# Kernel optimization log

Hardware: AMD Instinct MI355X
Metric: run time of the kernel (lower is better)

Reference implementation:

```python
import jax, jax.numpy as jnp
import numpy as np

B, L, D, K, MAXL = 2, 1024, 256, 64, 1024
EPS = 1e-5

def _encode(x, pos, w1, b1, w2, b2, wa, ba):
    # x: [B,L,D] -> complex phasors [B,L,K]
    xa = x + pos[: x.shape[1]][None]
    h = jax.nn.gelu(xa @ w1 + b1, approximate=False)
    phase = jnp.tanh(h @ w2 + b2) * np.float32(np.pi)
    amp = jax.nn.softplus(xa @ wa + ba) + np.float32(0.1)
    return (amp * jnp.exp(1j * phase)).astype(jnp.complex64)

def setup_inputs() -> dict:
    key = jax.random.key(0)
    ks = jax.random.split(key, 24)
    def lin_w(k, i, o):
        return (jax.random.normal(k, (i, o), jnp.float32) / np.sqrt(np.float32(i)))
    def pos(k):
        return jax.random.normal(k, (MAXL, D), jnp.float32) * np.float32(0.02)
    inp = {
        'x': jax.random.normal(ks[0], (B, L, D), jnp.float32),
        'pos_k': pos(ks[1]),
        'w1_k': lin_w(ks[2], D, D), 'b1_k': jnp.zeros((D,), jnp.float32),
        'w2_k': lin_w(ks[3], D, K), 'b2_k': jnp.zeros((K,), jnp.float32),
        'wa_k': lin_w(ks[4], D, K), 'ba_k': jnp.zeros((K,), jnp.float32),
        'pos_q': pos(ks[5]),
        'w1_q': lin_w(ks[6], D, D), 'b1_q': jnp.zeros((D,), jnp.float32),
        'w2_q': lin_w(ks[7], D, K), 'b2_q': jnp.zeros((K,), jnp.float32),
        'wa_q': lin_w(ks[8], D, K), 'ba_q': jnp.zeros((K,), jnp.float32),
        'wv': lin_w(ks[9], D, D), 'bv': jnp.zeros((D,), jnp.float32),
        'ln_g': jnp.ones((D,), jnp.float32), 'ln_b': jnp.zeros((D,), jnp.float32),
        'wo': lin_w(ks[10], D, D), 'bo': jnp.zeros((D,), jnp.float32),
    }
    return inp

def reference(x, pos_k, w1_k, b1_k, w2_k, b2_k, wa_k, ba_k,
              pos_q, w1_q, b1_q, w2_q, b2_q, wa_q, ba_q,
              wv, bv, ln_g, ln_b, wo, bo):
    Bx, Lx, Dx = x.shape
    kp = _encode(x, pos_k, w1_k, b1_k, w2_k, b2_k, wa_k, ba_k)  # [B,L,K] complex
    qp = _encode(x, pos_q, w1_q, b1_q, w2_q, b2_q, wa_q, ba_q)  # [B,L,K] complex
    V = (x @ wv + bv).astype(jnp.complex64)                      # [B,L,D]
    bound = kp[:, :, :, None] * V[:, :, None, :]                 # [B,L,K,D]
    memory = jnp.cumsum(bound, axis=1)                           # [B,L,K,D]
    retrieved = jnp.real(jnp.einsum('blkd,blk->bld', memory, jnp.conj(qp)))
    positions = jnp.arange(1, Lx + 1, dtype=jnp.float32)
    norm = jnp.sqrt(positions * np.float32(kp.shape[-1]))[None, :, None]
    r = retrieved / norm
    mu = jnp.mean(r, axis=-1, keepdims=True)
    var = jnp.var(r, axis=-1, keepdims=True)
    rn = (r - mu) / jnp.sqrt(var + np.float32(EPS)) * ln_g + ln_b
    return x + rn @ wo + bo
```

## Files before the change

kernel.cpp:

```cpp
#include <hip/hip_runtime.h>
#include <hip/hip_bf16.h>

typedef __attribute__((ext_vector_type(8))) short short8;
typedef __attribute__((ext_vector_type(4))) float float4v;

constexpr int B = 2, L = 1024, D = 256, K = 64;
constexpr int N = B * L;
constexpr int NC = L / 64;

constexpr int WT2_OFF = 524288;

__device__ __forceinline__ ushort bf16_hi(float v) {
  return (ushort)(__float_as_uint(v) >> 16);
}
__device__ __forceinline__ float hi_f(float v) {
  return __uint_as_float(__float_as_uint(v) & 0xFFFF0000u);
}
__device__ __forceinline__ ushort bf16_rne(float v) {
  uint b = __float_as_uint(v);
  b += 0x7FFF + ((b >> 16) & 1);
  return (ushort)(b >> 16);
}

__global__ __launch_bounds__(256) void prep_kernel(
    const float* __restrict__ w1_k, const float* __restrict__ w1_q,
    const float* __restrict__ wv, const float* __restrict__ wo,
    const float* __restrict__ w2_k, const float* __restrict__ wa_k,
    const float* __restrict__ w2_q, const float* __restrict__ wa_q,
    ushort* __restrict__ WT) {
  __shared__ float Lt[64][65];
  const int bi = blockIdx.x, tid = threadIdx.x;
  const float* src;
  int ncols, k0, n0;
  ushort* dhi;
  int losz;
  if (bi < 64) {
    const int m = bi >> 4, t = bi & 15;
    src = (m == 0) ? w1_k : (m == 1) ? w1_q : (m == 2) ? wv : wo;
    ncols = 256; k0 = (t >> 2) * 64; n0 = (t & 3) * 64;
    dhi = WT + m * 131072; losz = 65536;
  } else {
    const int m = (bi - 64) >> 2, kt = (bi - 64) & 3;
    src = (m == 0) ? w2_k : (m == 1) ? wa_k : (m == 2) ? w2_q : wa_q;
    ncols = 64; k0 = kt * 64; n0 = 0;
    dhi = WT + WT2_OFF + m * 32768; losz = 16384;
  }
  ushort* dlo = dhi + losz;
  for (int p = 0; p < 16; ++p) {
    const int kr = p * 4 + (tid >> 6), nc = tid & 63;
    Lt[kr][nc] = src[(k0 + kr) * ncols + n0 + nc];
  }
  __syncthreads();
  const int n = tid >> 2, kq = tid & 3;
  uint uh[8], ul[8];
  for (int i = 0; i < 8; ++i) {
    const float v0 = Lt[kq * 16 + 2 * i][n];
    const float v1 = Lt[kq * 16 + 2 * i + 1][n];
    uh[i] = (uint)bf16_hi(v0) | ((uint)bf16_hi(v1) << 16);
    ul[i] = (uint)bf16_rne(v0 - hi_f(v0)) | ((uint)bf16_rne(v1 - hi_f(v1)) << 16);
  }
  const int oidx = (n0 + n) * 256 + k0 + kq * 16;
  *(uint4*)&dhi[oidx] = make_uint4(uh[0], uh[1], uh[2], uh[3]);
  *(uint4*)&dhi[oidx + 8] = make_uint4(uh[4], uh[5], uh[6], uh[7]);
  *(uint4*)&dlo[oidx] = make_uint4(ul[0], ul[1], ul[2], ul[3]);
  *(uint4*)&dlo[oidx + 8] = make_uint4(ul[4], ul[5], ul[6], ul[7]);
}

__global__ __launch_bounds__(256) void enc1_kernel(
    const float* __restrict__ x, const float* __restrict__ pos_k,
    const float* __restrict__ pos_q,
    const float* __restrict__ b1_k, const float* __restrict__ b1_q,
    const float* __restrict__ bv, const ushort* __restrict__ WT,
    float* __restrict__ hk, float* __restrict__ hq, float* __restrict__ V) {
  __shared__ __align__(16) ushort Ah[32][40], Al[32][40];
  __shared__ __align__(16) ushort Bh[64][40], Bl[64][40];
  const int tid = threadIdx.x;
  const int g = blockIdx.x / 256;
  const int rem = blockIdx.x % 256;
  const int row0 = (rem >> 2) * 32, nb = (rem & 3) * 64;
  const float* pos = (g == 0) ? pos_k : (g == 1) ? pos_q : nullptr;
  const ushort* Wh = WT + g * 131072;
  const ushort* Wl = Wh + 65536;
  const int w = tid >> 6, lane = tid & 63;
  const int m16 = lane & 15, quad = lane >> 4;

  float4v acc[2] = {};

  for (int k0 = 0; k0 < 256; k0 += 32) {
    __syncthreads();
    {
      const int r = tid >> 3, kc = (tid & 7) * 4;
      const int row = row0 + r, l = row & (L - 1);
      float4 xv = *(const float4*)&x[row * D + k0 + kc];
      if (pos) {
        const float4 pv = *(const float4*)&pos[l * D + k0 + kc];
        xv.x += pv.x; xv.y += pv.y; xv.z += pv.z; xv.w += pv.w;
      }
      ushort4 h4, l4;
      h4.x = bf16_hi(xv.x); l4.x = bf16_rne(xv.x - hi_f(xv.x));
      h4.y = bf16_hi(xv.y); l4.y = bf16_rne(xv.y - hi_f(xv.y));
      h4.z = bf16_hi(xv.z); l4.z = bf16_rne(xv.z - hi_f(xv.z));
      h4.w = bf16_hi(xv.w); l4.w = bf16_rne(xv.w - hi_f(xv.w));
      *(ushort4*)&Ah[r][kc] = h4;
      *(ushort4*)&Al[r][kc] = l4;
    }
    {
      const int n = tid >> 2, chunk = tid & 3;
      const int ga = (nb + n) * 256 + k0 + chunk * 8;
      *(uint4*)&Bh[n][chunk * 8] = *(const uint4*)&Wh[ga];
      *(uint4*)&Bl[n][chunk * 8] = *(const uint4*)&Wl[ga];
    }
    __syncthreads();

    short8 afh[2], afl[2];
#pragma unroll
    for (int r = 0; r < 2; ++r) {
      afh[r] = *(const short8*)&Ah[r * 16 + m16][quad * 8];
      afl[r] = *(const short8*)&Al[r * 16 + m16][quad * 8];
    }
    const int col = w * 16 + m16;
    const short8 bfh = *(const short8*)&Bh[col][quad * 8];
    const short8 bfl = *(const short8*)&Bl[col][quad * 8];
#pragma unroll
    for (int r = 0; r < 2; ++r) {
      acc[r] = __builtin_amdgcn_mfma_f32_16x16x32_bf16(afh[r], bfh, acc[r], 0, 0, 0);
      acc[r] = __builtin_amdgcn_mfma_f32_16x16x32_bf16(afh[r], bfl, acc[r], 0, 0, 0);
      acc[r] = __builtin_amdgcn_mfma_f32_16x16x32_bf16(afl[r], bfh, acc[r], 0, 0, 0);
    }
  }

  float* outp = (g == 0) ? hk : (g == 1) ? hq : V;
  const float* bp = (g == 0) ? b1_k : (g == 1) ? b1_q : bv;
  const int colg = nb + w * 16 + m16;
  const float bias = bp[colg];
#pragma unroll
  for (int r = 0; r < 2; ++r)
#pragma unroll
    for (int j = 0; j < 4; ++j) {
      const int rowg = row0 + r * 16 + quad * 4 + j;
      float v = acc[r][j] + bias;
      if (g < 2) v = 0.5f * v * (1.0f + erff(v * 0.70710678f));
      outp[rowg * D + colg] = v;
    }
}

__global__ __launch_bounds__(512) void enc2_kernel(
    const float* __restrict__ x, const float* __restrict__ pos_k,
    const float* __restrict__ pos_q, const float* __restrict__ hk,
    const float* __restrict__ hq,
    const float* __restrict__ b2_k, const float* __restrict__ ba_k,
    const float* __restrict__ b2_q, const float* __restrict__ ba_q,
    const ushort* __restrict__ WT,
    float* __restrict__ kr, float* __restrict__ ki,
    float* __restrict__ qr, float* __restrict__ qi) {
  __shared__ __align__(16) ushort Ahh[16][40], Ahl[16][40], Axh[16][40], Axl[16][40];
  __shared__ __align__(16) ushort B2h[64][40], B2l[64][40], Bah[64][40], Bal[64][40];
  __shared__ float phL[16][68], amL[16][68];
  const int tid = threadIdx.x;
  const int e = blockIdx.x >> 7;
  const int r0g = (blockIdx.x & 127) * 16;
  const float* hsrc = e ? hq : hk;
  const float* pos = e ? pos_q : pos_k;
  const ushort* W2h = WT + WT2_OFF + (e ? 2 : 0) * 32768;
  const ushort* W2l = W2h + 16384;
  const ushort* Wah = WT + WT2_OFF + (e ? 3 : 1) * 32768;
  const ushort* Wal = Wah + 16384;
  const int w = tid >> 6, lane = tid & 63;
  const int m16 = lane & 15, quad = lane >> 4;
  const int mat = w & 1, ct = w >> 1;

  float4v acc = {};
  for (int k0 = 0; k0 < 256; k0 += 32) {
    __syncthreads();
    {
      const int half = tid >> 8;
      const int t2 = tid & 255;
      const int r = t2 >> 4, kc = (t2 & 15) * 2;
      const int row = r0g + r, l = row & (L - 1);
      if (half == 0) {
        const float2 hv = *(const float2*)&hsrc[row * D + k0 + kc];
        ushort2 h2, l2;
        h2.x = bf16_hi(hv.x); l2.x = bf16_rne(hv.x - hi_f(hv.x));
        h2.y = bf16_hi(hv.y); l2.y = bf16_rne(hv.y - hi_f(hv.y));
        *(ushort2*)&Ahh[r][kc] = h2;
        *(ushort2*)&Ahl[r][kc] = l2;
      } else {
        const float2 xv = *(const float2*)&x[row * D + k0 + kc];
        const float2 pv = *(const float2*)&pos[l * D + k0 + kc];
        const float a0 = xv.x + pv.x, a1 = xv.y + pv.y;
        ushort2 h2, l2;
        h2.x = bf16_hi(a0); l2.x = bf16_rne(a0 - hi_f(a0));
        h2.y = bf16_hi(a1); l2.y = bf16_rne(a1 - hi_f(a1));
        *(ushort2*)&Axh[r][kc] = h2;
        *(ushort2*)&Axl[r][kc] = l2;
      }
    }
    {
      const int sel = tid >> 7;
      const int idx = tid & 127;
      const int n = idx >> 1, ch = (idx & 1) * 2;
      const int ga = n * 256 + k0 + ch * 8;
      const ushort* s = (sel == 0) ? W2h : (sel == 1) ? W2l : (sel == 2) ? Wah : Wal;
      ushort* dst = (sel == 0) ? &B2h[n][ch * 8] : (sel == 1) ? &B2l[n][ch * 8]
                  : (sel == 2) ? &Bah[n][ch * 8] : &Bal[n][ch * 8];
      *(uint4*)dst = *(const uint4*)&s[ga];
      *(uint4*)(dst + 8) = *(const uint4*)&s[ga + 8];
    }
    __syncthreads();

    const short8 ah = mat ? *(const short8*)&Axh[m16][quad * 8]
                          : *(const short8*)&Ahh[m16][quad * 8];
    const short8 al = mat ? *(const short8*)&Axl[m16][quad * 8]
                          : *(const short8*)&Ahl[m16][quad * 8];
    const int col = ct * 16 + m16;
    const short8 bh = mat ? *(const short8*)&Bah[col][quad * 8]
                          : *(const short8*)&B2h[col][quad * 8];
    const short8 bl = mat ? *(const short8*)&Bal[col][quad * 8]
                          : *(const short8*)&B2l[col][quad * 8];
    acc = __builtin_amdgcn_mfma_f32_16x16x32_bf16(ah, bh, acc, 0, 0, 0);
    acc = __builtin_amdgcn_mfma_f32_16x16x32_bf16(ah, bl, acc, 0, 0, 0);
    acc = __builtin_amdgcn_mfma_f32_16x16x32_bf16(al, bh, acc, 0, 0, 0);
  }

  {
    const int colk = ct * 16 + m16;
    if (mat == 0) {
      const float b2v = (e ? b2_q : b2_k)[colk];
#pragma unroll
      for (int j = 0; j < 4; ++j)
        phL[quad * 4 + j][colk] = tanhf(acc[j] + b2v) * 3.14159265358979f;
    } else {
      const float bav = (e ? ba_q : ba_k)[colk];
#pragma unroll
      for (int j = 0; j < 4; ++j) {
        const float av = acc[j] + bav;
        amL[quad * 4 + j][colk] = fmaxf(av, 0.0f) + log1pf(expf(-fabsf(av))) + 0.1f;
      }
    }
  }
  __syncthreads();
  {
    float* pr = e ? qr : kr;
    float* pim = e ? qi : ki;
#pragma unroll
    for (int p = 0; p < 2; ++p) {
      const int idx = p * 512 + tid;
      const int r = idx >> 6, ccol = idx & 63;
      const int row = r0g + r;
      const float a = amL[r][ccol], pph = phL[r][ccol];
      pr[row * K + ccol] = a * cosf(pph);
      pim[row * K + ccol] = a * sinf(pph);
    }
  }
}

__global__ __launch_bounds__(256) void tbuild_kernel(
    const float* __restrict__ kr, const float* __restrict__ ki,
    const float* __restrict__ V, float* __restrict__ TMt) {
  const int id = blockIdx.x;
  const int dc = id & 15, c = (id >> 4) & 15, b = id >> 8;
  const int tid = threadIdx.x;
  const int n0 = b * L + c * 64;
  const int dl = tid & 15;
  const int kb = tid >> 4;

  __shared__ float krL[64][68], kiL[64][68];
  __shared__ float VL[64][20];
  __shared__ float Tl[16][204];
  for (int e = tid; e < 1024; e += 256) {
    const int t = e >> 4, k4 = (e & 15) * 4;
    *(float4*)&krL[t][k4] = *(const float4*)&kr[(n0 + t) * K + k4];
    *(float4*)&kiL[t][k4] = *(const float4*)&ki[(n0 + t) * K + k4];
  }
  {
    const int t = tid >> 2, f = (tid & 3) * 4;
    *(float4*)&VL[t][f] = *(const float4*)&V[(n0 + t) * D + dc * 16 + f];
  }
  __syncthreads();

  {
    const int t0 = (tid >> 4) * 4;
#pragma unroll
    for (int i = 0; i < 4; ++i) Tl[dl][128 + t0 + i] = VL[t0 + i][dl];
  }

  float ar[4] = {0.f, 0.f, 0.f, 0.f}, ai[4] = {0.f, 0.f, 0.f, 0.f};
#pragma unroll 4
  for (int t = 0; t < 64; ++t) {
    const float vt = VL[t][dl];
    const float4 k4r = *(const float4*)&krL[t][kb * 4];
    const float4 k4i = *(const float4*)&kiL[t][kb * 4];
    ar[0] += k4r.x * vt; ar[1] += k4r.y * vt; ar[2] += k4r.z * vt; ar[3] += k4r.w * vt;
    ai[0] += k4i.x * vt; ai[1] += k4i.y * vt; ai[2] += k4i.z * vt; ai[3] += k4i.w * vt;
  }

#pragma unroll
  for (int i = 0; i < 4; ++i) {
    Tl[dl][kb * 4 + i] = ar[i];
    Tl[dl][64 + kb * 4 + i] = ai[i];
  }
  __syncthreads();

  float* dst = &TMt[(((size_t)(b * 16 + c)) * 256 + dc * 16) * 192];
#pragma unroll
  for (int p = 0; p < 3; ++p) {
    const int e = p * 256 + tid;
    const int row = e / 48, f4 = e % 48;
    *(float4*)&dst[(size_t)row * 192 + f4 * 4] = *(const float4*)&Tl[row][f4 * 4];
  }
}

__global__ __launch_bounds__(512) void ret_kernel(
    const float* __restrict__ qr, const float* __restrict__ qi,
    const float* __restrict__ kr, const float* __restrict__ ki,
    const float* __restrict__ TMt, float* __restrict__ ret,
    float* __restrict__ LNred) {
  __shared__ __align__(16) ushort Ah[64][200], Al[64][200];
  __shared__ __align__(16) ushort Kh[64][136], Kl[64][136];
  __shared__ __align__(16) ushort Bh[32][200], Bl[32][200];
  const int tid = threadIdx.x;
  const int dc = blockIdx.x & 7;
  const int c = (blockIdx.x >> 3) & 15;
  const int b = blockIdx.x >> 7;
  const int n0 = b * L + c * 64;
  const int cols0 = dc * 32;
  const int w = tid >> 6, lane = tid & 63;
  const int m16 = lane & 15, quad = lane >> 4;

#pragma unroll
  for (int j = 0; j < 4; ++j) {
    const int e = j * 512 + tid;
    const int row = e >> 5, c4 = e & 31;
    const int col0 = (c4 & 15) * 4;
    const int acol = (c4 < 16 ? 0 : 64) + col0;
    {
      const float* src = (c4 < 16) ? qr : qi;
      const float4 v = *(const float4*)&src[(n0 + row) * K + col0];
      ushort4 h4, l4;
      h4.x = bf16_hi(v.x); l4.x = bf16_rne(v.x - hi_f(v.x));
      h4.y = bf16_hi(v.y); l4.y = bf16_rne(v.y - hi_f(v.y));
      h4.z = bf16_hi(v.z); l4.z = bf16_rne(v.z - hi_f(v.z));
      h4.w = bf16_hi(v.w); l4.w = bf16_rne(v.w - hi_f(v.w));
      *(ushort4*)&Ah[row][acol] = h4;
      *(ushort4*)&Al[row][acol] = l4;
    }
    {
      const float* src = (c4 < 16) ? kr : ki;
      const float4 v = *(const float4*)&src[(n0 + row) * K + col0];
      ushort4 h4, l4;
      h4.x = bf16_hi(v.x); l4.x = bf16_rne(v.x - hi_f(v.x));
      h4.y = bf16_hi(v.y); l4.y = bf16_rne(v.y - hi_f(v.y));
      h4.z = bf16_hi(v.z); l4.z = bf16_rne(v.z - hi_f(v.z));
      h4.w = bf16_hi(v.w); l4.w = bf16_rne(v.w - hi_f(v.w));
      *(ushort4*)&Kh[row][acol] = h4;
      *(ushort4*)&Kl[row][acol] = l4;
    }
  }

  float4 mac0 = {}, mac1 = {};
  {
    const int prow = tid >> 4, in0 = (tid & 15) * 8;
    const float* base = &TMt[(size_t)(b * 16) * 49152 +
                             (size_t)(cols0 + prow) * 192 + in0];
    for (int cp = 0; cp < c; ++cp) {
      const float* p = base + (size_t)cp * 49152;
      const float4 v0 = *(const float4*)p;
      const float4 v1 = *(const float4*)(p + 4);
      mac0.x += v0.x; mac0.y += v0.y; mac0.z += v0.z; mac0.w += v0.w;
      mac1.x += v1.x; mac1.y += v1.y; mac1.z += v1.z; mac1.w += v1.w;
    }
  }
  __syncthreads();

  {
    const int rt = w & 3;
    const int cp = (w >> 2) * 2;
    float4v sc[2] = {};
#pragma unroll
    for (int kk = 0; kk < 128; kk += 32) {
      const short8 ah = *(const short8*)&Ah[rt * 16 + m16][kk + quad * 8];
      const short8 al = *(const short8*)&Al[rt * 16 + m16][kk + quad * 8];
#pragma unroll
      for (int cc = 0; cc < 2; ++cc) {
        const int ct = cp + cc;
        const short8 bh = *(const short8*)&Kh[ct * 16 + m16][kk + quad * 8];
        const short8 bl = *(const short8*)&Kl[ct * 16 + m16][kk + quad * 8];
        sc[cc] = __builtin_amdgcn_mfma_f32_16x16x32_bf16(ah, bh, sc[cc], 0, 0, 0);
        sc[cc] = __builtin_amdgcn_mfma_f32_16x16x32_bf16(ah, bl, sc[cc], 0, 0, 0);
        sc[cc] = __builtin_amdgcn_mfma_f32_16x16x32_bf16(al, bh, sc[cc], 0, 0, 0);
      }
    }
#pragma unroll
    for (int cc = 0; cc < 2; ++cc)
#pragma unroll
      for (int j = 0; j < 4; ++j) {
        const int row = rt * 16 + quad * 4 + j;
        const int t = (cp + cc) * 16 + m16;
        const float s = (t <= row) ? sc[cc][j] : 0.0f;
        Ah[row][128 + t] = bf16_hi(s);
        Al[row][128 + t] = bf16_rne(s - hi_f(s));
      }
  }

  {
    const int prow = tid >> 4, in0 = (tid & 15) * 8;
    ushort4 h4, l4;
    h4.x = bf16_hi(mac0.x); l4.x = bf16_rne(mac0.x - hi_f(mac0.x));
    h4.y = bf16_hi(mac0.y); l4.y = bf16_rne(mac0.y - hi_f(mac0.y));
    h4.z = bf16_hi(mac0.z); l4.z = bf16_rne(mac0.z - hi_f(mac0.z));
    h4.w = bf16_hi(mac0.w); l4.w = bf16_rne(mac0.w - hi_f(mac0.w));
    *(ushort4*)&Bh[prow][in0] = h4;
    *(ushort4*)&Bl[prow][in0] = l4;
    h4.x = bf16_hi(mac1.x); l4.x = bf16_rne(mac1.x - hi_f(mac1.x));
    h4.y = bf16_hi(mac1.y); l4.y = bf16_rne(mac1.y - hi_f(mac1.y));
    h4.z = bf16_hi(mac1.z); l4.z = bf16_rne(mac1.z - hi_f(mac1.z));
    h4.w = bf16_hi(mac1.w); l4.w = bf16_rne(mac1.w - hi_f(mac1.w));
    *(ushort4*)&Bh[prow][in0 + 4] = h4;
    *(ushort4*)&Bl[prow][in0 + 4] = l4;

    const int vrow = tid >> 4, vin = 128 + (tid & 15) * 4;
    const float4 v = *(const float4*)&TMt[(size_t)(b * 16 + c) * 49152 +
                                          (size_t)(cols0 + vrow) * 192 + vin];
    ushort4 vh, vl;
    vh.x = bf16_hi(v.x); vl.x = bf16_rne(v.x - hi_f(v.x));
    vh.y = bf16_hi(v.y); vl.y = bf16_rne(v.y - hi_f(v.y));
    vh.z = bf16_hi(v.z); vl.z = bf16_rne(v.z - hi_f(v.z));
    vh.w = bf16_hi(v.w); vl.w = bf16_rne(v.w - hi_f(v.w));
    *(ushort4*)&Bh[vrow][vin] = vh;
    *(ushort4*)&Bl[vrow][vin] = vl;
  }
  __syncthreads();

  {
    const int rt = w & 3;
    const int ct = w >> 2;
    float4v r2 = {};
#pragma unroll
    for (int kk = 0; kk < 6; ++kk) {
      const short8 ah = *(const short8*)&Ah[rt * 16 + m16][kk * 32 + quad * 8];
      const short8 al = *(const short8*)&Al[rt * 16 + m16][kk * 32 + quad * 8];
      const short8 bh = *(const short8*)&Bh[ct * 16 + m16][kk * 32 + quad * 8];
      const short8 bl = *(const short8*)&Bl[ct * 16 + m16][kk * 32 + quad * 8];
      r2 = __builtin_amdgcn_mfma_f32_16x16x32_bf16(ah, bh, r2, 0, 0, 0);
      r2 = __builtin_amdgcn_mfma_f32_16x16x32_bf16(ah, bl, r2, 0, 0, 0);
      r2 = __builtin_amdgcn_mfma_f32_16x16x32_bf16(al, bh, r2, 0, 0, 0);
    }
#pragma unroll
    for (int j = 0; j < 4; ++j) {
      const int rowL = rt * 16 + quad * 4 + j;
      const float nrm = rsqrtf((float)(c * 64 + rowL + 1) * 64.0f);
      const float v = r2[j] * nrm;
      ret[(size_t)(n0 + rowL) * D + cols0 + ct * 16 + m16] = v;
      float sj = v, s2j = v * v;
      for (int off = 1; off < 16; off <<= 1) {
        sj += __shfl_xor(sj, off, 64);
        s2j += __shfl_xor(s2j, off, 64);
      }
      if (m16 == 0) {
        LNred[(size_t)(n0 + rowL) * 32 + (dc * 2 + ct) * 2 + 0] = sj;
        LNred[(size_t)(n0 + rowL) * 32 + (dc * 2 + ct) * 2 + 1] = s2j;
      }
    }
  }
}

__global__ __launch_bounds__(512) void out2_kernel(
    const float* __restrict__ ret, const float* __restrict__ LNred,
    const float* __restrict__ x, const float* __restrict__ ln_g,
    const float* __restrict__ ln_b, const ushort* __restrict__ WT,
    const float* __restrict__ bo, float* __restrict__ out) {
  __shared__ __align__(16) ushort Ah[32][40], Al[32][40];
  __shared__ __align__(16) ushort Bh[64][40], Bl[64][40];
  __shared__ float mu_s[32], rs_s[32];
  const int tid = threadIdx.x;
  const int row0 = (blockIdx.x >> 2) * 32, nb = (blockIdx.x & 3) * 64;
  const ushort* Wh = WT + 3 * 131072;
  const ushort* Wl = Wh + 65536;
  const int w = tid >> 6, lane = tid & 63;
  const int m16 = lane & 15, quad = lane >> 4;
  const int rt = w & 1, cq = w >> 1;

  if (tid < 32) {
    const int row = row0 + tid;
    float s = 0.f, s2 = 0.f;
#pragma unroll
    for (int i = 0; i < 16; ++i) {
      s += LNred[(size_t)row * 32 + i * 2 + 0];
      s2 += LNred[(size_t)row * 32 + i * 2 + 1];
    }
    const float mu = s * (1.0f / 256.0f);
    mu_s[tid] = mu;
    rs_s[tid] = rsqrtf(s2 * (1.0f / 256.0f) - mu * mu + 1e-5f);
  }

  float4v acc = {};
  for (int k0 = 0; k0 < 256; k0 += 32) {
    __syncthreads();
    {
      const int r = tid >> 4, kc = (tid & 15) * 2;
      const float2 v = *(const float2*)&ret[(size_t)(row0 + r) * D + k0 + kc];
      const float2 g2 = *(const float2*)&ln_g[k0 + kc];
      const float2 b2 = *(const float2*)&ln_b[k0 + kc];
      const float mu = mu_s[r], rs = rs_s[r];
      const float a0 = (v.x - mu) * rs * g2.x + b2.x;
      const float a1 = (v.y - mu) * rs * g2.y + b2.y;
      ushort2 h2, l2;
      h2.x = bf16_hi(a0); l2.x = bf16_rne(a0 - hi_f(a0));
      h2.y = bf16_hi(a1); l2.y = bf16_rne(a1 - hi_f(a1));
      *(ushort2*)&Ah[r][kc] = h2;
      *(ushort2*)&Al[r][kc] = l2;
    }
    {
      const int plane = tid >> 8;
      const int n = (tid >> 2) & 63, chunk = tid & 3;
      const int ga = (nb + n) * 256 + k0 + chunk * 8;
      if (plane == 0) *(uint4*)&Bh[n][chunk * 8] = *(const uint4*)&Wh[ga];
      else            *(uint4*)&Bl[n][chunk * 8] = *(const uint4*)&Wl[ga];
    }
    __syncthreads();

    const short8 afh = *(const short8*)&Ah[rt * 16 + m16][quad * 8];
    const short8 afl = *(const short8*)&Al[rt * 16 + m16][quad * 8];
    const int col = cq * 16 + m16;
    const short8 bfh = *(const short8*)&Bh[col][quad * 8];
    const short8 bfl = *(const short8*)&Bl[col][quad * 8];
    acc = __builtin_amdgcn_mfma_f32_16x16x32_bf16(afh, bfh, acc, 0, 0, 0);
    acc = __builtin_amdgcn_mfma_f32_16x16x32_bf16(afh, bfl, acc, 0, 0, 0);
    acc = __builtin_amdgcn_mfma_f32_16x16x32_bf16(afl, bfh, acc, 0, 0, 0);
  }

  const int colg = nb + cq * 16 + m16;
  const float bias = bo[colg];
#pragma unroll
  for (int j = 0; j < 4; ++j) {
    const int rowg = row0 + rt * 16 + quad * 4 + j;
    out[rowg * D + colg] = x[rowg * D + colg] + acc[j] + bias;
  }
}

extern "C" void kernel_launch(void* const* d_in, const int* in_sizes, int n_in,
                              void* d_out, int out_size, void* d_ws, size_t ws_size,
                              hipStream_t stream) {
  (void)in_sizes; (void)n_in; (void)out_size; (void)ws_size;
  const float* x    = (const float*)d_in[0];
  const float* pos_k= (const float*)d_in[1];
  const float* w1_k = (const float*)d_in[2];
  const float* b1_k = (const float*)d_in[3];
  const float* w2_k = (const float*)d_in[4];
  const float* b2_k = (const float*)d_in[5];
  const float* wa_k = (const float*)d_in[6];
  const float* ba_k = (const float*)d_in[7];
  const float* pos_q= (const float*)d_in[8];
  const float* w1_q = (const float*)d_in[9];
  const float* b1_q = (const float*)d_in[10];
  const float* w2_q = (const float*)d_in[11];
  const float* b2_q = (const float*)d_in[12];
  const float* wa_q = (const float*)d_in[13];
  const float* ba_q = (const float*)d_in[14];
  const float* wv   = (const float*)d_in[15];
  const float* bv   = (const float*)d_in[16];
  const float* ln_g = (const float*)d_in[17];
  const float* ln_b = (const float*)d_in[18];
  const float* wo   = (const float*)d_in[19];
  const float* bo   = (const float*)d_in[20];

  float* ws = (float*)d_ws;
  float* kr = ws;
  float* ki = kr + (size_t)N * K;
  float* qr = ki + (size_t)N * K;
  float* qi = qr + (size_t)N * K;
  float* V  = qi + (size_t)N * K;
  float* TMt = V + (size_t)N * D;
  float* ret = TMt + (size_t)B * NC * 256 * 192;
  float* LNred = ret + (size_t)N * D;
  float* hk = LNred + (size_t)N * 32;
  float* hq = hk + (size_t)N * D;
  ushort* WT = (ushort*)(hq + (size_t)N * D);

  prep_kernel<<<80, 256, 0, stream>>>(w1_k, w1_q, wv, wo,
                                      w2_k, wa_k, w2_q, wa_q, WT);
  enc1_kernel<<<768, 256, 0, stream>>>(x, pos_k, pos_q, b1_k, b1_q, bv, WT,
                                       hk, hq, V);
  enc2_kernel<<<256, 512, 0, stream>>>(x, pos_k, pos_q, hk, hq,
                                       b2_k, ba_k, b2_q, ba_q, WT,
                                       kr, ki, qr, qi);
  tbuild_kernel<<<B * NC * 16, 256, 0, stream>>>(kr, ki, V, TMt);
  ret_kernel<<<B * NC * 8, 512, 0, stream>>>(qr, qi, kr, ki, TMt, ret, LNred);
  out2_kernel<<<256, 512, 0, stream>>>(ret, LNred, x, ln_g, ln_b, WT, bo,
                                       (float*)d_out);
}
```

Measured before the change: 148.3 us.

## Split retrieval and output kernels into smaller blocks and trim score precision

The retrieval kernel now runs 256-thread blocks that each own 16 output columns instead of 32, which doubles the grid. Each wave computes a full 16x64 score tile. The score buffer is stored in a single bf16 plane, which drops its low-order correction term and its MFMA pass. The K staging buffer and the prefix-memory buffer share one LDS region, separated by an extra barrier, to cut shared-memory use. The output projection kernel also moves to 256-thread blocks with 32-column tiles and float4 LayerNorm staging. Together these aim to raise occupancy and parallelism, at the cost of recomputing the Q/K scores in twice as many blocks and some loss of accuracy in the score matrix.

```diff
diff --git a/kernel.cpp b/kernel.cpp
--- a/kernel.cpp
+++ b/kernel.cpp
@@ -310,26 +310,31 @@
   }
 }
 
-__global__ __launch_bounds__(512) void ret_kernel(
+__global__ __launch_bounds__(256) void ret_kernel(
     const float* __restrict__ qr, const float* __restrict__ qi,
     const float* __restrict__ kr, const float* __restrict__ ki,
     const float* __restrict__ TMt, float* __restrict__ ret,
     float* __restrict__ LNred) {
-  __shared__ __align__(16) ushort Ah[64][200], Al[64][200];
-  __shared__ __align__(16) ushort Kh[64][136], Kl[64][136];
-  __shared__ __align__(16) ushort Bh[32][200], Bl[32][200];
+  __shared__ __align__(16) ushort Qh[64][136], Ql[64][136];
+  __shared__ __align__(16) ushort Sh[64][72];
+  __shared__ __align__(16) char KB[34816];
+  ushort* Kh = (ushort*)KB;
+  ushort* Kl = Kh + 64 * 136;
+  ushort* Bh = (ushort*)KB;
+  ushort* Bl = Bh + 16 * 200;
+
   const int tid = threadIdx.x;
-  const int dc = blockIdx.x & 7;
-  const int c = (blockIdx.x >> 3) & 15;
-  const int b = blockIdx.x >> 7;
+  const int dc = blockIdx.x & 15;
+  const int c = (blockIdx.x >> 4) & 15;
+  const int b = blockIdx.x >> 8;
   const int n0 = b * L + c * 64;
-  const int cols0 = dc * 32;
+  const int cols0 = dc * 16;
   const int w = tid >> 6, lane = tid & 63;
   const int m16 = lane & 15, quad = lane >> 4;
 
 #pragma unroll
-  for (int j = 0; j < 4; ++j) {
-    const int e = j * 512 + tid;
+  for (int j = 0; j < 8; ++j) {
+    const int e = j * 256 + tid;
     const int row = e >> 5, c4 = e & 31;
     const int col0 = (c4 & 15) * 4;
     const int acol = (c4 < 16 ? 0 : 64) + col0;
@@ -341,8 +346,8 @@
       h4.y = bf16_hi(v.y); l4.y = bf16_rne(v.y - hi_f(v.y));
       h4.z = bf16_hi(v.z); l4.z = bf16_rne(v.z - hi_f(v.z));
       h4.w = bf16_hi(v.w); l4.w = bf16_rne(v.w - hi_f(v.w));
-      *(ushort4*)&Ah[row][acol] = h4;
-      *(ushort4*)&Al[row][acol] = l4;
+      *(ushort4*)&Qh[row][acol] = h4;
+      *(ushort4*)&Ql[row][acol] = l4;
     }
     {
       const float* src = (c4 < 16) ? kr : ki;
@@ -352,8 +357,8 @@
       h4.y = bf16_hi(v.y); l4.y = bf16_rne(v.y - hi_f(v.y));
       h4.z = bf16_hi(v.z); l4.z = bf16_rne(v.z - hi_f(v.z));
       h4.w = bf16_hi(v.w); l4.w = bf16_rne(v.w - hi_f(v.w));
-      *(ushort4*)&Kh[row][acol] = h4;
-      *(ushort4*)&Kl[row][acol] = l4;
+      *(ushort4*)&Kh[row * 136 + acol] = h4;
+      *(ushort4*)&Kl[row * 136 + acol] = l4;
     }
   }
 
@@ -373,34 +378,30 @@
   __syncthreads();
 
   {
-    const int rt = w & 3;
-    const int cp = (w >> 2) * 2;
-    float4v sc[2] = {};
+    float4v sc[4] = {};
 #pragma unroll
     for (int kk = 0; kk < 128; kk += 32) {
-      const short8 ah = *(const short8*)&Ah[rt * 16 + m16][kk + quad * 8];
-      const short8 al = *(const short8*)&Al[rt * 16 + m16][kk + quad * 8];
-#pragma unroll
-      for (int cc = 0; cc < 2; ++cc) {
-        const int ct = cp + cc;
-        const short8 bh = *(const short8*)&Kh[ct * 16 + m16][kk + quad * 8];
-        const short8 bl = *(const short8*)&Kl[ct * 16 + m16][kk + quad * 8];
-        sc[cc] = __builtin_amdgcn_mfma_f32_16x16x32_bf16(ah, bh, sc[cc], 0, 0, 0);
-        sc[cc] = __builtin_amdgcn_mfma_f32_16x16x32_bf16(ah, bl, sc[cc], 0, 0, 0);
-        sc[cc] = __builtin_amdgcn_mfma_f32_16x16x32_bf16(al, bh, sc[cc], 0, 0, 0);
+      const short8 ah = *(const short8*)&Qh[w * 16 + m16][kk + quad * 8];
+      const short8 al = *(const short8*)&Ql[w * 16 + m16][kk + quad * 8];
+#pragma unroll
+      for (int ct = 0; ct < 4; ++ct) {
+        const short8 bh = *(const short8*)&Kh[(ct * 16 + m16) * 136 + kk + quad * 8];
+        const short8 bl = *(const short8*)&Kl[(ct * 16 + m16) * 136 + kk + quad * 8];
+        sc[ct] = __builtin_amdgcn_mfma_f32_16x16x32_bf16(ah, bh, sc[ct], 0, 0, 0);
+        sc[ct] = __builtin_amdgcn_mfma_f32_16x16x32_bf16(ah, bl, sc[ct], 0, 0, 0);
+        sc[ct] = __builtin_amdgcn_mfma_f32_16x16x32_bf16(al, bh, sc[ct], 0, 0, 0);
       }
     }
 #pragma unroll
-    for (int cc = 0; cc < 2; ++cc)
+    for (int ct = 0; ct < 4; ++ct)
 #pragma unroll
       for (int j = 0; j < 4; ++j) {
-        const int row = rt * 16 + quad * 4 + j;
-        const int t = (cp + cc) * 16 + m16;
-        const float s = (t <= row) ? sc[cc][j] : 0.0f;
-        Ah[row][128 + t] = bf16_hi(s);
-        Al[row][128 + t] = bf16_rne(s - hi_f(s));
+        const int row = w * 16 + quad * 4 + j;
+        const int t = ct * 16 + m16;
+        Sh[row][t] = (t <= row) ? bf16_hi(sc[ct][j]) : (ushort)0;
       }
   }
+  __syncthreads();
 
   {
     const int prow = tid >> 4, in0 = (tid & 15) * 8;
@@ -409,14 +410,14 @@
     h4.y = bf16_hi(mac0.y); l4.y = bf16_rne(mac0.y - hi_f(mac0.y));
     h4.z = bf16_hi(mac0.z); l4.z = bf16_rne(mac0.z - hi_f(mac0.z));
     h4.w = bf16_hi(mac0.w); l4.w = bf16_rne(mac0.w - hi_f(mac0.w));
-    *(ushort4*)&Bh[prow][in0] = h4;
-    *(ushort4*)&Bl[prow][in0] = l4;
+    *(ushort4*)&Bh[prow * 200 + in0] = h4;
+    *(ushort4*)&Bl[prow * 200 + in0] = l4;
     h4.x = bf16_hi(mac1.x); l4.x = bf16_rne(mac1.x - hi_f(mac1.x));
     h4.y = bf16_hi(mac1.y); l4.y = bf16_rne(mac1.y - hi_f(mac1.y));
     h4.z = bf16_hi(mac1.z); l4.z = bf16_rne(mac1.z - hi_f(mac1.z));
     h4.w = bf16_hi(mac1.w); l4.w = bf16_rne(mac1.w - hi_f(mac1.w));
-    *(ushort4*)&Bh[prow][in0 + 4] = h4;
-    *(ushort4*)&Bl[prow][in0 + 4] = l4;
+    *(ushort4*)&Bh[prow * 200 + in0 + 4] = h4;
+    *(ushort4*)&Bl[prow * 200 + in0 + 4] = l4;
 
     const int vrow = tid >> 4, vin = 128 + (tid & 15) * 4;
     const float4 v = *(const float4*)&TMt[(size_t)(b * 16 + c) * 49152 +
@@ -426,54 +427,60 @@
     vh.y = bf16_hi(v.y); vl.y = bf16_rne(v.y - hi_f(v.y));
     vh.z = bf16_hi(v.z); vl.z = bf16_rne(v.z - hi_f(v.z));
     vh.w = bf16_hi(v.w); vl.w = bf16_rne(v.w - hi_f(v.w));
-    *(ushort4*)&Bh[vrow][vin] = vh;
-    *(ushort4*)&Bl[vrow][vin] = vl;
+    *(ushort4*)&Bh[vrow * 200 + vin] = vh;
+    *(ushort4*)&Bl[vrow * 200 + vin] = vl;
   }
   __syncthreads();
 
   {
-    const int rt = w & 3;
-    const int ct = w >> 2;
     float4v r2 = {};
 #pragma unroll
-    for (int kk = 0; kk < 6; ++kk) {
-      const short8 ah = *(const short8*)&Ah[rt * 16 + m16][kk * 32 + quad * 8];
-      const short8 al = *(const short8*)&Al[rt * 16 + m16][kk * 32 + quad * 8];
-      const short8 bh = *(const short8*)&Bh[ct * 16 + m16][kk * 32 + quad * 8];
-      const short8 bl = *(const short8*)&Bl[ct * 16 + m16][kk * 32 + quad * 8];
+    for (int kk = 0; kk < 4; ++kk) {
+      const short8 ah = *(const short8*)&Qh[w * 16 + m16][kk * 32 + quad * 8];
+      const short8 al = *(const short8*)&Ql[w * 16 + m16][kk * 32 + quad * 8];
+      const short8 bh = *(const short8*)&Bh[m16 * 200 + kk * 32 + quad * 8];
+      const short8 bl = *(const short8*)&Bl[m16 * 200 + kk * 32 + quad * 8];
       r2 = __builtin_amdgcn_mfma_f32_16x16x32_bf16(ah, bh, r2, 0, 0, 0);
       r2 = __builtin_amdgcn_mfma_f32_16x16x32_bf16(ah, bl, r2, 0, 0, 0);
       r2 = __builtin_amdgcn_mfma_f32_16x16x32_bf16(al, bh, r2, 0, 0, 0);
     }
 #pragma unroll
+    for (int s2 = 0; s2 < 2; ++s2) {
+      const short8 ah = *(const short8*)&Sh[w * 16 + m16][s2 * 32 + quad * 8];
+      const short8 bh = *(const short8*)&Bh[m16 * 200 + 128 + s2 * 32 + quad * 8];
+      const short8 bl = *(const short8*)&Bl[m16 * 200 + 128 + s2 * 32 + quad * 8];
+      r2 = __builtin_amdgcn_mfma_f32_16x16x32_bf16(ah, bh, r2, 0, 0, 0);
+      r2 = __builtin_amdgcn_mfma_f32_16x16x32_bf16(ah, bl, r2, 0, 0, 0);
+    }
+#pragma unroll
     for (int j = 0; j < 4; ++j) {
-      const int rowL = rt * 16 + quad * 4 + j;
+      const int rowL = w * 16 + quad * 4 + j;
       const float nrm = rsqrtf((float)(c * 64 + rowL + 1) * 64.0f);
       const float v = r2[j] * nrm;
-      ret[(size_t)(n0 + rowL) * D + cols0 + ct * 16 + m16] = v;
+      ret[(size_t)(n0 + rowL) * D + cols0 + m16] = v;
       float sj = v, s2j = v * v;
       for (int off = 1; off < 16; off <<= 1) {
         sj += __shfl_xor(sj, off, 64);
         s2j += __shfl_xor(s2j, off, 64);
       }
       if (m16 == 0) {
-        LNred[(size_t)(n0 + rowL) * 32 + (dc * 2 + ct) * 2 + 0] = sj;
-        LNred[(size_t)(n0 + rowL) * 32 + (dc * 2 + ct) * 2 + 1] = s2j;
+        LNred[(size_t)(n0 + rowL) * 32 + dc * 2 + 0] = sj;
+        LNred[(size_t)(n0 + rowL) * 32 + dc * 2 + 1] = s2j;
       }
     }
   }
 }
 
-__global__ __launch_bounds__(512) void out2_kernel(
+__global__ __launch_bounds__(256) void out2_kernel(
     const float* __restrict__ ret, const float* __restrict__ LNred,
     const float* __restrict__ x, const float* __restrict__ ln_g,
     const float* __restrict__ ln_b, const ushort* __restrict__ WT,
     const float* __restrict__ bo, float* __restrict__ out) {
   __shared__ __align__(16) ushort Ah[32][40], Al[32][40];
-  __shared__ __align__(16) ushort Bh[64][40], Bl[64][40];
+  __shared__ __align__(16) ushort Bh[32][40], Bl[32][40];
   __shared__ float mu_s[32], rs_s[32];
   const int tid = threadIdx.x;
-  const int row0 = (blockIdx.x >> 2) * 32, nb = (blockIdx.x & 3) * 64;
+  const int row0 = (blockIdx.x >> 3) * 32, nb = (blockIdx.x & 7) * 32;
   const ushort* Wh = WT + 3 * 131072;
   const ushort* Wl = Wh + 65536;
   const int w = tid >> 6, lane = tid & 63;
@@ -497,22 +504,27 @@
   for (int k0 = 0; k0 < 256; k0 += 32) {
     __syncthreads();
     {
-      const int r = tid >> 4, kc = (tid & 15) * 2;
-      const float2 v = *(const float2*)&ret[(size_t)(row0 + r) * D + k0 + kc];
-      const float2 g2 = *(const float2*)&ln_g[k0 + kc];
-      const float2 b2 = *(const float2*)&ln_b[k0 + kc];
+      const int r = tid >> 3, kc = (tid & 7) * 4;
+      const float4 v = *(const float4*)&ret[(size_t)(row0 + r) * D + k0 + kc];
+      const float4 g4 = *(const float4*)&ln_g[k0 + kc];
+      const float4 b4 = *(const float4*)&ln_b[k0 + kc];
       const float mu = mu_s[r], rs = rs_s[r];
-      const float a0 = (v.x - mu) * rs * g2.x + b2.x;
-      const float a1 = (v.y - mu) * rs * g2.y + b2.y;
-      ushort2 h2, l2;
-      h2.x = bf16_hi(a0); l2.x = bf16_rne(a0 - hi_f(a0));
-      h2.y = bf16_hi(a1); l2.y = bf16_rne(a1 - hi_f(a1));
-      *(ushort2*)&Ah[r][kc] = h2;
-      *(ushort2*)&Al[r][kc] = l2;
-    }
-    {
-      const int plane = tid >> 8;
-      const int n = (tid >> 2) & 63, chunk = tid & 3;
+      float a0 = (v.x - mu) * rs * g4.x + b4.x;
+      float a1 = (v.y - mu) * rs * g4.y + b4.y;
+      float a2 = (v.z - mu) * rs * g4.z + b4.z;
+      float a3 = (v.w - mu) * rs * g4.w + b4.w;
+      ushort4 h4, l4;
+      h4.x = bf16_hi(a0); l4.x = bf16_rne(a0 - hi_f(a0));
+      h4.y = bf16_hi(a1); l4.y = bf16_rne(a1 - hi_f(a1));
+      h4.z = bf16_hi(a2); l4.z = bf16_rne(a2 - hi_f(a2));
+      h4.w = bf16_hi(a3); l4.w = bf16_rne(a3 - hi_f(a3));
+      *(ushort4*)&Ah[r][kc] = h4;
+      *(ushort4*)&Al[r][kc] = l4;
+    }
+    {
+      const int plane = tid >> 7;
+      const int idx = tid & 127;
+      const int n = idx >> 2, chunk = idx & 3;
       const int ga = (nb + n) * 256 + k0 + chunk * 8;
       if (plane == 0) *(uint4*)&Bh[n][chunk * 8] = *(const uint4*)&Wh[ga];
       else            *(uint4*)&Bl[n][chunk * 8] = *(const uint4*)&Wl[ga];
@@ -585,7 +597,7 @@
                                        b2_k, ba_k, b2_q, ba_q, WT,
                                        kr, ki, qr, qi);
   tbuild_kernel<<<B * NC * 16, 256, 0, stream>>>(kr, ki, V, TMt);
-  ret_kernel<<<B * NC * 8, 512, 0, stream>>>(qr, qi, kr, ki, TMt, ret, LNred);
-  out2_kernel<<<256, 512, 0, stream>>>(ret, LNred, x, ln_g, ln_b, WT, bo,
+  ret_kernel<<<B * NC * 16, 256, 0, stream>>>(qr, qi, kr, ki, TMt, ret, LNred);
+  out2_kernel<<<512, 256, 0, stream>>>(ret, LNred, x, ln_g, ln_b, WT, bo,
                                        (float*)d_out);
 }
```

Result: no change. 145.8 us (-1.7%).
